# Performance work log

Measured on AMD Instinct MI355X. Metric: run time of the kernel, lower is better.

## Reference

```python
import jax, jax.numpy as jnp
import numpy as np

B, S, D = 1, 2048, 4096
H, KV, HD = 32, 8, 128          # n_heads, n_kv_heads, head_dim
NREP = H // KV                  # 4
SCALE = 1.0 / np.sqrt(HD).astype(np.float32)
ROPE_THETA = 10000.0


def setup_inputs() -> dict:
    key = jax.random.key(0)
    kx, kq, kk, kv, ko = jax.random.split(key, 5)
    x = jax.random.normal(kx, (B, S, D), jnp.float32)
    # precomputed rotary embeddings: (S, HD//2, 2) = (cos, sin)
    inv_freq = 1.0 / (ROPE_THETA ** (np.arange(0, HD, 2, dtype=np.float64) / HD))
    ang = np.outer(np.arange(S, dtype=np.float64), inv_freq)
    freqs_cis = jnp.asarray(np.stack([np.cos(ang), np.sin(ang)], axis=-1), jnp.float32)
    # additive causal mask
    mask = jnp.triu(jnp.full((S, S), -1e9, jnp.float32), k=1)
    std = 0.02
    wq = jax.random.normal(kq, (H * HD, D), jnp.float32) * std   # torch Linear layout (out, in)
    wk = jax.random.normal(kk, (KV * HD, D), jnp.float32) * std
    wv = jax.random.normal(kv, (KV * HD, D), jnp.float32) * std
    wo = jax.random.normal(ko, (D, H * HD), jnp.float32) * std
    return {"x": x, "freqs_cis": freqs_cis, "mask": mask,
            "wq": wq, "wk": wk, "wv": wv, "wo": wo}


def _apply_rope(t, fc):
    # t: [B, S, h, HD]; fc: [S, HD//2, 2] (cos, sin). Pairs adjacent dims as complex.
    b, s, h, hd = t.shape
    tr = t.reshape(b, s, h, hd // 2, 2)
    cos = fc[None, :, None, :, 0]
    sin = fc[None, :, None, :, 1]
    re = tr[..., 0] * cos - tr[..., 1] * sin
    im = tr[..., 0] * sin + tr[..., 1] * cos
    return jnp.stack([re, im], axis=-1).reshape(b, s, h, hd)


def reference(x, freqs_cis, mask, wq, wk, wv, wo):
    q = (x @ wq.T).reshape(B, S, H, HD)
    k = (x @ wk.T).reshape(B, S, KV, HD)
    v = (x @ wv.T).reshape(B, S, KV, HD)
    q = _apply_rope(q, freqs_cis)
    k = _apply_rope(k, freqs_cis)
    # GQA: head h = g * NREP + r attends to kv group g (same math as repeat_kv)
    qg = q.reshape(B, S, KV, NREP, HD)
    scores = jnp.einsum('bsgrd,btgd->bgrst', qg, k) * SCALE  # [B,KV,NREP,S,S]
    scores = scores + mask
    probs = jax.nn.softmax(scores.astype(jnp.float32), axis=-1).astype(q.dtype)
    out = jnp.einsum('bgrst,btgd->bsgrd', probs, v).reshape(B, S, H * HD)
    return out @ wo.T
```

## Files before the change

kernel.cpp:

```cpp
#include <hip/hip_runtime.h>
#include <stdint.h>

#define SCALE_F 0.08838834764831845f
#define LOG2E_F 1.4426950408889634f
#define QS_F (SCALE_F * LOG2E_F)

typedef __bf16 bf16x8_t __attribute__((ext_vector_type(8)));
typedef unsigned short u16x8 __attribute__((ext_vector_type(8)));
typedef float f32x4 __attribute__((ext_vector_type(4)));
typedef float f32x16 __attribute__((ext_vector_type(16)));

__device__ __forceinline__ unsigned short f2bf(float f) {
  unsigned int u = __float_as_uint(f);
  unsigned int r = ((u >> 16) & 1u) + 0x7FFFu;
  return (unsigned short)((u + r) >> 16);
}
__device__ __forceinline__ float bf2f(unsigned short s) {
  return __uint_as_float(((unsigned int)s) << 16);
}
__device__ __forceinline__ f32x4 mfma16(u16x8 a, u16x8 b, f32x4 c) {
  return __builtin_amdgcn_mfma_f32_16x16x32_bf16(
      __builtin_bit_cast(bf16x8_t, a), __builtin_bit_cast(bf16x8_t, b), c, 0, 0, 0);
}
__device__ __forceinline__ f32x16 mfma32(u16x8 a, u16x8 b, f32x16 c) {
  return __builtin_amdgcn_mfma_f32_32x32x16_bf16(
      __builtin_bit_cast(bf16x8_t, a), __builtin_bit_cast(bf16x8_t, b), c, 0, 0, 0);
}
__device__ __forceinline__ unsigned int cvtpk(float lo, float hi) {
  unsigned int r;
  asm("v_cvt_pk_bf16_f32 %0, %1, %2" : "=v"(r) : "v"(lo), "v"(hi));
  return r;
}
__device__ __forceinline__ float exp2_hw(float x) {
  float r;
  asm("v_exp_f32 %0, %1" : "=v"(r) : "v"(x));
  return r;
}
__device__ __forceinline__ void gload_lds16(const void* g, void* l) {
  __builtin_amdgcn_global_load_lds((const __attribute__((address_space(1))) void*)g,
                                   (__attribute__((address_space(3))) void*)l, 16, 0, 0);
}

__global__ void cvt_all(const float* __restrict__ x, const float* __restrict__ wq,
                        const float* __restrict__ wk, const float* __restrict__ wv,
                        const float* __restrict__ wo, unsigned short* __restrict__ xb,
                        unsigned short* __restrict__ wfus, unsigned short* __restrict__ wob) {
  const size_t M = 1024 * 1024;
  int b = blockIdx.x;
  const float* src;
  unsigned short* dst;
  int rb;
  if (b < 4096)       { src = x;  dst = xb;            rb = b; }
  else if (b < 12288) { src = wq; dst = wfus;          rb = b - 4096; }
  else if (b < 14336) { src = wk; dst = wfus + 16 * M; rb = b - 12288; }
  else if (b < 16384) { src = wv; dst = wfus + 20 * M; rb = b - 14336; }
  else                { src = wo; dst = wob;           rb = b - 16384; }
  size_t i = (size_t)rb * 2048 + threadIdx.x * 8;
  float4 v0 = *(const float4*)(src + i);
  float4 v1 = *(const float4*)(src + i + 4);
  uint4 o;
  o.x = (unsigned int)f2bf(v0.x) | ((unsigned int)f2bf(v0.y) << 16);
  o.y = (unsigned int)f2bf(v0.z) | ((unsigned int)f2bf(v0.w) << 16);
  o.z = (unsigned int)f2bf(v1.x) | ((unsigned int)f2bf(v1.y) << 16);
  o.w = (unsigned int)f2bf(v1.z) | ((unsigned int)f2bf(v1.w) << 16);
  *(uint4*)(dst + i) = o;
}

__global__ void kvtile(const unsigned short* __restrict__ QKV, const float* __restrict__ fc,
                       unsigned short* __restrict__ Ktil, unsigned short* __restrict__ Vtil) {
  __shared__ unsigned short vlds[32 * 128];
  int b0 = blockIdx.x;
  int tid = threadIdx.x;
  if (b0 < 512) {
    int b = b0, kvg = b >> 6, kvt = b & 63;
#pragma unroll
    for (int cc = 0; cc < 2; ++cc) {
      int c = tid + cc * 256;
      int s = c >> 5, r = c & 31;
      int key = kvt * 32 + r;
      u16x8 v = *(const u16x8*)&QKV[(size_t)key * 6144 + 4096 + kvg * 128 + s * 8];
      unsigned int o[4];
#pragma unroll
      for (int t = 0; t < 4; ++t) {
        int m = s * 4 + t;
        float cs = fc[(key * 64 + m) * 2];
        float sn = fc[(key * 64 + m) * 2 + 1];
        float a = bf2f((unsigned short)v[2 * t]), bb = bf2f((unsigned short)v[2 * t + 1]);
        o[t] = (unsigned int)f2bf(a * cs - bb * sn) |
               ((unsigned int)f2bf(a * sn + bb * cs) << 16);
      }
      *(uint4*)&Ktil[(size_t)b * 4096 + c * 8] = make_uint4(o[0], o[1], o[2], o[3]);
    }
  } else {
    int b = b0 - 512, kvg = b >> 6, kvt = b & 63;
#pragma unroll
    for (int cc = 0; cc < 2; ++cc) {
      int cl = tid + cc * 256;
      int r = cl >> 4, q = cl & 15;
      *(uint4*)&vlds[r * 128 + q * 8] =
          *(const uint4*)&QKV[(size_t)(kvt * 32 + r) * 6144 + 5120 + kvg * 128 + q * 8];
    }
    __syncthreads();
#pragma unroll
    for (int cc = 0; cc < 2; ++cc) {
      int c = tid + cc * 256;
      int v = c >> 7, hd = c & 127;
      unsigned short o[8];
#pragma unroll
      for (int t = 0; t < 8; ++t) o[t] = vlds[(v * 8 + t) * 128 + hd];
      *(uint4*)&Vtil[(size_t)b * 4096 + c * 8] = *(uint4*)o;
    }
  }
}

__global__ __launch_bounds__(512, 2) void gemm_qkv(const unsigned short* __restrict__ A,
                                                   const unsigned short* __restrict__ BT,
                                                   unsigned short* __restrict__ C) {
  const int K = 4096, N = 6144;
  __shared__ __align__(16) unsigned short smem[2 * 28672];
  const int tid = threadIdx.x;
  const int w = tid >> 6, l = tid & 63;
  const int wm = w >> 2, wn = w & 3;
  const int c16 = l & 15, h4 = l >> 4;
  const int wg = ((int)blockIdx.x & 7) * 32 + ((int)blockIdx.x >> 3);
  const int m0 = (wg & 7) << 8, n0 = (wg >> 3) * 192;

  int growA[4], gcolA[4], growB[3], gcolB[3];
#pragma unroll
  for (int p = 0; p < 4; ++p) {
    int c = p * 512 + tid, ll = c & 63;
    growA[p] = ((c >> 6) & 15) * 16 + (ll & 15);
    gcolA[p] = (c >> 10) * 32 + ((ll >> 4) << 3);
  }
#pragma unroll
  for (int p = 0; p < 3; ++p) {
    int c = p * 512 + tid, ll = c & 63, f6 = c >> 6;
    int kc = (f6 >= 12) ? 1 : 0;
    growB[p] = (f6 - 12 * kc) * 16 + (ll & 15);
    gcolB[p] = kc * 32 + ((ll >> 4) << 3);
  }
  auto stageA = [&](int e, int ks, int p) {
    gload_lds16(A + (size_t)(m0 + growA[p]) * K + ks + gcolA[p],
                &smem[e * 28672 + (p * 512 + tid) * 8]);
  };
  auto stageB = [&](int e, int ks, int p) {
    gload_lds16(BT + (size_t)(n0 + growB[p]) * K + ks + gcolB[p],
                &smem[e * 28672 + 16384 + (p * 512 + tid) * 8]);
  };

  f32x4 acc[2][4][3];
#pragma unroll
  for (int mh = 0; mh < 2; ++mh)
#pragma unroll
    for (int mf = 0; mf < 4; ++mf)
#pragma unroll
      for (int nf = 0; nf < 3; ++nf)
#pragma unroll
        for (int r = 0; r < 4; ++r) acc[mh][mf][nf][r] = 0.f;

  stageA(0, 0, 0); stageA(0, 0, 1); stageB(0, 0, 0); stageB(0, 0, 1);
  stageA(0, 0, 2); stageA(0, 0, 3); stageB(0, 0, 2);
  asm volatile("s_waitcnt vmcnt(3)" ::: "memory");
  __builtin_amdgcn_sched_barrier(0);
  asm volatile("s_barrier" ::: "memory");

  const int nt = K >> 6;
  u16x8 bfr[3];
  for (int t = 0; t < nt; ++t) {
    const int d = t & 1, e = d ^ 1;
    const int dA = d * 28672, dB = dA + 16384;
    const int ks = ((t + 1 < nt) ? t + 1 : t) << 6;
#pragma unroll
    for (int p = 0; p < 4; ++p) {
      const int kc = p >> 1, mh = p & 1;
      u16x8 af[4];
#pragma unroll
      for (int mf = 0; mf < 4; ++mf)
        af[mf] = *(const u16x8*)&smem[dA + ((kc * 16 + wm * 8 + mh * 4 + mf) * 64 + l) * 8];
      if (mh == 0) {
#pragma unroll
        for (int nf = 0; nf < 3; ++nf)
          bfr[nf] = *(const u16x8*)&smem[dB + ((kc * 12 + wn * 3 + nf) * 64 + l) * 8];
      }
      if (p == 0)      { stageA(e, ks, 0); stageA(e, ks, 1); }
      else if (p == 1) { stageB(e, ks, 0); stageB(e, ks, 1); }
      else if (p == 2) { stageA(e, ks, 2); stageA(e, ks, 3); }
      else             { stageB(e, ks, 2); }
      asm volatile("s_barrier" ::: "memory");
      asm volatile("s_waitcnt lgkmcnt(0)" ::: "memory");
      __builtin_amdgcn_sched_barrier(0);
      __builtin_amdgcn_s_setprio(1);
#pragma unroll
      for (int mf = 0; mf < 4; ++mf)
#pragma unroll
        for (int nf = 0; nf < 3; ++nf)
          acc[mh][mf][nf] = mfma16(af[mf], bfr[nf], acc[mh][mf][nf]);
      __builtin_amdgcn_s_setprio(0);
      __builtin_amdgcn_sched_barrier(0);
      if (p == 1) asm volatile("s_waitcnt vmcnt(4)" ::: "memory");
      else if (p == 3) asm volatile("s_waitcnt vmcnt(3)" ::: "memory");
      asm volatile("s_barrier" ::: "memory");
    }
  }
  asm volatile("s_waitcnt vmcnt(0)" ::: "memory");

#pragma unroll
  for (int mh = 0; mh < 2; ++mh)
#pragma unroll
    for (int mf = 0; mf < 4; ++mf)
#pragma unroll
      for (int nf = 0; nf < 3; ++nf)
#pragma unroll
        for (int r = 0; r < 4; ++r) {
          int row = m0 + wm * 128 + mh * 64 + mf * 16 + h4 * 4 + r;
          int col = n0 + wn * 48 + nf * 16 + c16;
          C[(size_t)row * N + col] = f2bf(acc[mh][mf][nf][r]);
        }
}

__global__ __launch_bounds__(512, 2) void gemm_o(const unsigned short* __restrict__ A,
                                                 const unsigned short* __restrict__ BT,
                                                 float* __restrict__ C) {
  const int K = 4096, N = 4096;
  __shared__ __align__(16) unsigned short smem[2 * 24576];
  const int tid = threadIdx.x;
  const int w = tid >> 6, l = tid & 63;
  const int wm = w >> 2, wn = w & 3;
  const int c16 = l & 15, h4 = l >> 4;
  const int wg = ((int)blockIdx.x & 7) * 32 + ((int)blockIdx.x >> 3);
  const int m0 = (wg & 15) << 7, n0 = (wg >> 4) << 8;

  int growA[2], gcolA[2], growB[4], gcolB[4];
#pragma unroll
  for (int p = 0; p < 2; ++p) {
    int c = p * 512 + tid, ll = c & 63;
    growA[p] = ((c >> 6) & 7) * 16 + (ll & 15);
    gcolA[p] = (c >> 9) * 32 + ((ll >> 4) << 3);
  }
#pragma unroll
  for (int p = 0; p < 4; ++p) {
    int c = p * 512 + tid, ll = c & 63;
    growB[p] = ((c >> 6) & 15) * 16 + (ll & 15);
    gcolB[p] = (c >> 10) * 32 + ((ll >> 4) << 3);
  }
  auto stageA = [&](int e, int ks, int p) {
    gload_lds16(A + (size_t)(m0 + growA[p]) * K + ks + gcolA[p],
                &smem[e * 24576 + (p * 512 + tid) * 8]);
  };
  auto stageB = [&](int e, int ks, int p) {
    gload_lds16(BT + (size_t)(n0 + growB[p]) * K + ks + gcolB[p],
                &smem[e * 24576 + 8192 + (p * 512 + tid) * 8]);
  };

  f32x4 acc[4][4];
#pragma unroll
  for (int mf = 0; mf < 4; ++mf)
#pragma unroll
    for (int nc = 0; nc < 4; ++nc)
#pragma unroll
      for (int r = 0; r < 4; ++r) acc[mf][nc][r] = 0.f;

  stageA(0, 0, 0); stageB(0, 0, 0); stageB(0, 0, 1);
  stageA(0, 0, 1); stageB(0, 0, 2); stageB(0, 0, 3);
  asm volatile("s_waitcnt vmcnt(3)" ::: "memory");
  __builtin_amdgcn_sched_barrier(0);
  asm volatile("s_barrier" ::: "memory");

  const int nt = K >> 6;
  u16x8 af[4];
  for (int t = 0; t < nt; ++t) {
    const int d = t & 1, e = d ^ 1;
    const int dA = d * 24576, dB = dA + 8192;
    const int ks = ((t + 1 < nt) ? t + 1 : t) << 6;
#pragma unroll
    for (int p = 0; p < 4; ++p) {
      const int kc = p >> 1, nh = p & 1;
      if (nh == 0) {
#pragma unroll
        for (int mf = 0; mf < 4; ++mf)
          af[mf] = *(const u16x8*)&smem[dA + ((kc * 8 + wm * 4 + mf) * 64 + l) * 8];
      }
      u16x8 bfr[2];
#pragma unroll
      for (int nf = 0; nf < 2; ++nf)
        bfr[nf] = *(const u16x8*)&smem[dB + ((kc * 16 + wn * 4 + nh * 2 + nf) * 64 + l) * 8];
      if (p == 0)      { stageA(e, ks, 0); stageB(e, ks, 0); }
      else if (p == 1) { stageB(e, ks, 1); }
      else if (p == 2) { stageA(e, ks, 1); stageB(e, ks, 2); }
      else             { stageB(e, ks, 3); }
      asm volatile("s_barrier" ::: "memory");
      asm volatile("s_waitcnt lgkmcnt(0)" ::: "memory");
      __builtin_amdgcn_sched_barrier(0);
      __builtin_amdgcn_s_setprio(1);
#pragma unroll
      for (int mf = 0; mf < 4; ++mf)
#pragma unroll
        for (int nf = 0; nf < 2; ++nf)
          acc[mf][nh * 2 + nf] = mfma16(af[mf], bfr[nf], acc[mf][nh * 2 + nf]);
      __builtin_amdgcn_s_setprio(0);
      __builtin_amdgcn_sched_barrier(0);
      if (p == 1 || p == 3) asm volatile("s_waitcnt vmcnt(3)" ::: "memory");
      asm volatile("s_barrier" ::: "memory");
    }
  }
  asm volatile("s_waitcnt vmcnt(0)" ::: "memory");

#pragma unroll
  for (int mf = 0; mf < 4; ++mf)
#pragma unroll
    for (int nc = 0; nc < 4; ++nc)
#pragma unroll
      for (int r = 0; r < 4; ++r) {
        int row = m0 + wm * 64 + mf * 16 + h4 * 4 + r;
        int col = n0 + wn * 64 + nc * 16 + c16;
        C[(size_t)row * N + col] = acc[mf][nc][r];
      }
}

__global__ __launch_bounds__(256) void attnk(const unsigned short* __restrict__ Q,
                                             const float* __restrict__ fc,
                                             const unsigned short* __restrict__ Ktil,
                                             const unsigned short* __restrict__ Vtil,
                                             unsigned short* __restrict__ Ao) {
  __shared__ __align__(16) unsigned short Kbuf[2][4096];
  __shared__ __align__(16) unsigned short Vbuf[2][4096];
  const int tid = threadIdx.x;
  const int w = tid >> 6, l = tid & 63;
  const int q31 = l & 31, hi = l >> 5;
  const int b = blockIdx.x;
  const int kvg = b & 7;
  const int qg = 63 - (b >> 3);
  const int head = kvg * 4 + w;
  const int qrow = qg * 32 + q31;

  u16x8 qf[8];
#pragma unroll
  for (int kc = 0; kc < 8; ++kc) {
    u16x8 raw = *(const u16x8*)&Q[(size_t)qrow * 6144 + head * 128 + kc * 16 + hi * 8];
    int mi = qrow * 64 + kc * 8 + hi * 4;
    float4 cA = *(const float4*)&fc[(size_t)mi * 2];
    float4 cB = *(const float4*)&fc[(size_t)mi * 2 + 4];
    float cs[4] = {cA.x, cA.z, cB.x, cB.z};
    float sn[4] = {cA.y, cA.w, cB.y, cB.w};
    union { unsigned int u[4]; u16x8 v; } pk;
#pragma unroll
    for (int j = 0; j < 4; ++j) {
      float a = bf2f((unsigned short)raw[2 * j]);
      float bb = bf2f((unsigned short)raw[2 * j + 1]);
      pk.u[j] = (unsigned int)f2bf((a * cs[j] - bb * sn[j]) * QS_F) |
                ((unsigned int)f2bf((a * sn[j] + bb * cs[j]) * QS_F) << 16);
    }
    qf[kc] = pk.v;
  }

  f32x16 accO[4];
#pragma unroll
  for (int f = 0; f < 4; ++f)
#pragma unroll
    for (int r = 0; r < 16; ++r) accO[f][r] = 0.f;
  float m_run = -1e30f, l_run = 0.f;

  const unsigned short* ktb = Ktil + (size_t)kvg * 64 * 4096;
  const unsigned short* vtb = Vtil + (size_t)kvg * 64 * 4096;
  auto STAGE = [&](int d, int t) {
    const unsigned short* ks = ktb + (size_t)t * 4096 + w * 1024 + l * 8;
    const unsigned short* vs = vtb + (size_t)t * 4096 + w * 1024 + l * 8;
    gload_lds16(ks, &Kbuf[d][w * 1024 + l * 8]);
    gload_lds16(ks + 512, &Kbuf[d][w * 1024 + 512 + l * 8]);
    gload_lds16(vs, &Vbuf[d][w * 1024 + l * 8]);
    gload_lds16(vs + 512, &Vbuf[d][w * 1024 + 512 + l * 8]);
  };

  STAGE(0, 0);
  int cur = 0;
  for (int kvt = 0; kvt <= qg; ++kvt) {
    __builtin_amdgcn_s_barrier();
    __builtin_amdgcn_sched_barrier(0);
    if (kvt < qg) {
      STAGE(cur ^ 1, kvt + 1);
      asm volatile("s_waitcnt vmcnt(4)" ::: "memory");
    } else {
      asm volatile("s_waitcnt vmcnt(0)" ::: "memory");
    }
    __builtin_amdgcn_s_barrier();
    __builtin_amdgcn_sched_barrier(0);

    f32x16 s;
#pragma unroll
    for (int r = 0; r < 16; ++r) s[r] = 0.f;
#pragma unroll
    for (int kc = 0; kc < 8; ++kc) {
      u16x8 kf = *(const u16x8*)&Kbuf[cur][((2 * kc + hi) * 32 + q31) * 8];
      s = mfma32(kf, qf[kc], s);
    }

    if (kvt == qg) {
#pragma unroll
      for (int r = 0; r < 16; ++r) {
        int key = (r & 3) + 8 * (r >> 2) + 4 * hi;
        if (key > q31) s[r] = -1e30f;
      }
    }

    float pm = s[0];
#pragma unroll
    for (int r = 1; r < 16; ++r) pm = fmaxf(pm, s[r]);
    pm = fmaxf(pm, __shfl_xor(pm, 32, 64));
    if (!__all(pm - m_run <= 8.f)) {
      float mn = fmaxf(m_run, pm);
      float al = exp2_hw(m_run - mn);
      m_run = mn;
      l_run *= al;
#pragma unroll
      for (int f = 0; f < 4; ++f)
#pragma unroll
        for (int r = 0; r < 16; ++r) accO[f][r] *= al;
    }
    float p[16], ls = 0.f;
#pragma unroll
    for (int r = 0; r < 16; ++r) { p[r] = exp2_hw(s[r] - m_run); ls += p[r]; }
    l_run += ls + __shfl_xor(ls, 32, 64);

    unsigned int wv[8], wp[8];
#pragma unroll
    for (int i = 0; i < 8; ++i) wv[i] = cvtpk(p[2 * i], p[2 * i + 1]);
#pragma unroll
    for (int i = 0; i < 8; ++i) wp[i] = (unsigned int)__shfl_xor((int)wv[i], 32, 64);
    union { unsigned int u[4]; u16x8 v; } pf0, pf1;
    pf0.u[0] = hi ? wp[2] : wv[0];
    pf0.u[1] = hi ? wp[3] : wv[1];
    pf0.u[2] = hi ? wv[2] : wp[0];
    pf0.u[3] = hi ? wv[3] : wp[1];
    pf1.u[0] = hi ? wp[6] : wv[4];
    pf1.u[1] = hi ? wp[7] : wv[5];
    pf1.u[2] = hi ? wv[6] : wp[4];
    pf1.u[3] = hi ? wv[7] : wp[5];

#pragma unroll
    for (int f = 0; f < 4; ++f) {
      u16x8 vf0 = *(const u16x8*)&Vbuf[cur][((hi) * 128 + f * 32 + q31) * 8];
      u16x8 vf1 = *(const u16x8*)&Vbuf[cur][((2 + hi) * 128 + f * 32 + q31) * 8];
      accO[f] = mfma32(vf0, pf0.v, accO[f]);
      accO[f] = mfma32(vf1, pf1.v, accO[f]);
    }
    cur ^= 1;
  }

  float linv = 1.0f / l_run;
  unsigned short* orow = Ao + (size_t)qrow * 4096 + head * 128;
#pragma unroll
  for (int f = 0; f < 4; ++f)
#pragma unroll
    for (int g4 = 0; g4 < 4; ++g4) {
      unsigned int lo = (unsigned int)f2bf(accO[f][g4 * 4 + 0] * linv) |
                        ((unsigned int)f2bf(accO[f][g4 * 4 + 1] * linv) << 16);
      unsigned int hi2 = (unsigned int)f2bf(accO[f][g4 * 4 + 2] * linv) |
                         ((unsigned int)f2bf(accO[f][g4 * 4 + 3] * linv) << 16);
      *(uint2*)(orow + f * 32 + 8 * g4 + 4 * hi) = make_uint2(lo, hi2);
    }
}

extern "C" void kernel_launch(void* const* d_in, const int* in_sizes, int n_in,
                              void* d_out, int out_size, void* d_ws, size_t ws_size,
                              hipStream_t stream) {
  (void)in_sizes; (void)n_in; (void)out_size; (void)ws_size;
  const float* x  = (const float*)d_in[0];
  const float* fc = (const float*)d_in[1];
  const float* wq = (const float*)d_in[3];
  const float* wk = (const float*)d_in[4];
  const float* wv = (const float*)d_in[5];
  const float* wo = (const float*)d_in[6];

  const size_t M = 1024 * 1024;
  unsigned short* xb   = (unsigned short*)d_ws;
  unsigned short* wfus = xb   + 8 * M;
  unsigned short* wob  = wfus + 24 * M;
  unsigned short* QKV  = wob  + 16 * M;
  unsigned short* Ktil = QKV  + 12 * M;
  unsigned short* Vtil = Ktil + 2 * M;
  unsigned short* Ab   = xb;

  cvt_all<<<dim3(24576), 256, 0, stream>>>(x, wq, wk, wv, wo, xb, wfus, wob);

  gemm_qkv<<<dim3(256), 512, 0, stream>>>(xb, wfus, QKV);

  kvtile<<<dim3(1024), 256, 0, stream>>>(QKV, fc, Ktil, Vtil);

  attnk<<<dim3(512), 256, 0, stream>>>(QKV, fc, Ktil, Vtil, Ab);

  gemm_o<<<dim3(256), 512, 0, stream>>>(Ab, wob, (float*)d_out);
}
```

Before: 342.8 us.

## Process two KV tiles per pipeline stage and interleave causal block ordering

Result: faster. 328.4 us (-4.2%).

```diff
diff --git a/kernel.cpp b/kernel.cpp
--- a/kernel.cpp
+++ b/kernel.cpp
@@ -322,14 +322,15 @@
                                              const unsigned short* __restrict__ Ktil,
                                              const unsigned short* __restrict__ Vtil,
                                              unsigned short* __restrict__ Ao) {
-  __shared__ __align__(16) unsigned short Kbuf[2][4096];
-  __shared__ __align__(16) unsigned short Vbuf[2][4096];
+  __shared__ __align__(16) unsigned short Kbuf[2][8192];
+  __shared__ __align__(16) unsigned short Vbuf[2][8192];
   const int tid = threadIdx.x;
   const int w = tid >> 6, l = tid & 63;
   const int q31 = l & 31, hi = l >> 5;
   const int b = blockIdx.x;
   const int kvg = b & 7;
-  const int qg = 63 - (b >> 3);
+  const int j = b >> 3;
+  const int qg = (j < 32) ? (63 - 2 * j) : (2 * (j - 32));
   const int head = kvg * 4 + w;
   const int qrow = qg * 32 + q31;
 
@@ -344,11 +345,11 @@
     float sn[4] = {cA.y, cA.w, cB.y, cB.w};
     union { unsigned int u[4]; u16x8 v; } pk;
 #pragma unroll
-    for (int j = 0; j < 4; ++j) {
-      float a = bf2f((unsigned short)raw[2 * j]);
-      float bb = bf2f((unsigned short)raw[2 * j + 1]);
-      pk.u[j] = (unsigned int)f2bf((a * cs[j] - bb * sn[j]) * QS_F) |
-                ((unsigned int)f2bf((a * sn[j] + bb * cs[j]) * QS_F) << 16);
+    for (int jj = 0; jj < 4; ++jj) {
+      float a = bf2f((unsigned short)raw[2 * jj]);
+      float bb = bf2f((unsigned short)raw[2 * jj + 1]);
+      pk.u[jj] = (unsigned int)f2bf((a * cs[jj] - bb * sn[jj]) * QS_F) |
+                 ((unsigned int)f2bf((a * sn[jj] + bb * cs[jj]) * QS_F) << 16);
     }
     qf[kc] = pk.v;
   }
@@ -362,49 +363,67 @@
 
   const unsigned short* ktb = Ktil + (size_t)kvg * 64 * 4096;
   const unsigned short* vtb = Vtil + (size_t)kvg * 64 * 4096;
-  auto STAGE = [&](int d, int t) {
-    const unsigned short* ks = ktb + (size_t)t * 4096 + w * 1024 + l * 8;
-    const unsigned short* vs = vtb + (size_t)t * 4096 + w * 1024 + l * 8;
-    gload_lds16(ks, &Kbuf[d][w * 1024 + l * 8]);
-    gload_lds16(ks + 512, &Kbuf[d][w * 1024 + 512 + l * 8]);
-    gload_lds16(vs, &Vbuf[d][w * 1024 + l * 8]);
-    gload_lds16(vs + 512, &Vbuf[d][w * 1024 + 512 + l * 8]);
+  auto STAGE = [&](int d, int s) {
+    const unsigned short* ks = ktb + (size_t)s * 8192 + w * 2048 + l * 8;
+    const unsigned short* vs = vtb + (size_t)s * 8192 + w * 2048 + l * 8;
+#pragma unroll
+    for (int q = 0; q < 4; ++q) {
+      gload_lds16(ks + q * 512, &Kbuf[d][w * 2048 + q * 512 + l * 8]);
+      gload_lds16(vs + q * 512, &Vbuf[d][w * 2048 + q * 512 + l * 8]);
+    }
   };
 
+  const int nst = (qg >> 1) + 1;
   STAGE(0, 0);
   int cur = 0;
-  for (int kvt = 0; kvt <= qg; ++kvt) {
+  for (int st = 0; st < nst; ++st) {
     __builtin_amdgcn_s_barrier();
     __builtin_amdgcn_sched_barrier(0);
-    if (kvt < qg) {
-      STAGE(cur ^ 1, kvt + 1);
-      asm volatile("s_waitcnt vmcnt(4)" ::: "memory");
+    if (st + 1 < nst) {
+      STAGE(cur ^ 1, st + 1);
+      asm volatile("s_waitcnt vmcnt(8)" ::: "memory");
     } else {
       asm volatile("s_waitcnt vmcnt(0)" ::: "memory");
     }
     __builtin_amdgcn_s_barrier();
     __builtin_amdgcn_sched_barrier(0);
 
-    f32x16 s;
-#pragma unroll
-    for (int r = 0; r < 16; ++r) s[r] = 0.f;
+    f32x16 s0, s1;
+#pragma unroll
+    for (int r = 0; r < 16; ++r) { s0[r] = 0.f; s1[r] = 0.f; }
 #pragma unroll
     for (int kc = 0; kc < 8; ++kc) {
       u16x8 kf = *(const u16x8*)&Kbuf[cur][((2 * kc + hi) * 32 + q31) * 8];
-      s = mfma32(kf, qf[kc], s);
-    }
-
-    if (kvt == qg) {
-#pragma unroll
-      for (int r = 0; r < 16; ++r) {
-        int key = (r & 3) + 8 * (r >> 2) + 4 * hi;
-        if (key > q31) s[r] = -1e30f;
-      }
-    }
-
-    float pm = s[0];
-#pragma unroll
-    for (int r = 1; r < 16; ++r) pm = fmaxf(pm, s[r]);
+      s0 = mfma32(kf, qf[kc], s0);
+    }
+#pragma unroll
+    for (int kc = 0; kc < 8; ++kc) {
+      u16x8 kf = *(const u16x8*)&Kbuf[cur][4096 + ((2 * kc + hi) * 32 + q31) * 8];
+      s1 = mfma32(kf, qf[kc], s1);
+    }
+
+    if (st == nst - 1) {
+      if ((qg & 1) == 0) {
+#pragma unroll
+        for (int r = 0; r < 16; ++r) {
+          int key = (r & 3) + 8 * (r >> 2) + 4 * hi;
+          if (key > q31) s0[r] = -1e30f;
+          s1[r] = -1e30f;
+        }
+      } else {
+#pragma unroll
+        for (int r = 0; r < 16; ++r) {
+          int key = (r & 3) + 8 * (r >> 2) + 4 * hi;
+          if (key > q31) s1[r] = -1e30f;
+        }
+      }
+    }
+
+    float pm = s0[0];
+#pragma unroll
+    for (int r = 1; r < 16; ++r) pm = fmaxf(pm, s0[r]);
+#pragma unroll
+    for (int r = 0; r < 16; ++r) pm = fmaxf(pm, s1[r]);
     pm = fmaxf(pm, __shfl_xor(pm, 32, 64));
     if (!__all(pm - m_run <= 8.f)) {
       float mn = fmaxf(m_run, pm);
@@ -416,33 +435,61 @@
 #pragma unroll
         for (int r = 0; r < 16; ++r) accO[f][r] *= al;
     }
-    float p[16], ls = 0.f;
-#pragma unroll
-    for (int r = 0; r < 16; ++r) { p[r] = exp2_hw(s[r] - m_run); ls += p[r]; }
-    l_run += ls + __shfl_xor(ls, 32, 64);
-
-    unsigned int wv[8], wp[8];
-#pragma unroll
-    for (int i = 0; i < 8; ++i) wv[i] = cvtpk(p[2 * i], p[2 * i + 1]);
-#pragma unroll
-    for (int i = 0; i < 8; ++i) wp[i] = (unsigned int)__shfl_xor((int)wv[i], 32, 64);
-    union { unsigned int u[4]; u16x8 v; } pf0, pf1;
-    pf0.u[0] = hi ? wp[2] : wv[0];
-    pf0.u[1] = hi ? wp[3] : wv[1];
-    pf0.u[2] = hi ? wv[2] : wp[0];
-    pf0.u[3] = hi ? wv[3] : wp[1];
-    pf1.u[0] = hi ? wp[6] : wv[4];
-    pf1.u[1] = hi ? wp[7] : wv[5];
-    pf1.u[2] = hi ? wv[6] : wp[4];
-    pf1.u[3] = hi ? wv[7] : wp[5];
-
-#pragma unroll
-    for (int f = 0; f < 4; ++f) {
-      u16x8 vf0 = *(const u16x8*)&Vbuf[cur][((hi) * 128 + f * 32 + q31) * 8];
-      u16x8 vf1 = *(const u16x8*)&Vbuf[cur][((2 + hi) * 128 + f * 32 + q31) * 8];
-      accO[f] = mfma32(vf0, pf0.v, accO[f]);
-      accO[f] = mfma32(vf1, pf1.v, accO[f]);
-    }
+
+    float lsum = 0.f;
+    {
+      float p[16];
+#pragma unroll
+      for (int r = 0; r < 16; ++r) { p[r] = exp2_hw(s0[r] - m_run); lsum += p[r]; }
+      unsigned int wv[8], wp[8];
+#pragma unroll
+      for (int i = 0; i < 8; ++i) wv[i] = cvtpk(p[2 * i], p[2 * i + 1]);
+#pragma unroll
+      for (int i = 0; i < 8; ++i) wp[i] = (unsigned int)__shfl_xor((int)wv[i], 32, 64);
+      union { unsigned int u[4]; u16x8 v; } pf0, pf1;
+      pf0.u[0] = hi ? wp[2] : wv[0];
+      pf0.u[1] = hi ? wp[3] : wv[1];
+      pf0.u[2] = hi ? wv[2] : wp[0];
+      pf0.u[3] = hi ? wv[3] : wp[1];
+      pf1.u[0] = hi ? wp[6] : wv[4];
+      pf1.u[1] = hi ? wp[7] : wv[5];
+      pf1.u[2] = hi ? wv[6] : wp[4];
+      pf1.u[3] = hi ? wv[7] : wp[5];
+#pragma unroll
+      for (int f = 0; f < 4; ++f) {
+        u16x8 vf0 = *(const u16x8*)&Vbuf[cur][((hi) * 128 + f * 32 + q31) * 8];
+        u16x8 vf1 = *(const u16x8*)&Vbuf[cur][((2 + hi) * 128 + f * 32 + q31) * 8];
+        accO[f] = mfma32(vf0, pf0.v, accO[f]);
+        accO[f] = mfma32(vf1, pf1.v, accO[f]);
+      }
+    }
+    {
+      float p[16];
+#pragma unroll
+      for (int r = 0; r < 16; ++r) { p[r] = exp2_hw(s1[r] - m_run); lsum += p[r]; }
+      unsigned int wv[8], wp[8];
+#pragma unroll
+      for (int i = 0; i < 8; ++i) wv[i] = cvtpk(p[2 * i], p[2 * i + 1]);
+#pragma unroll
+      for (int i = 0; i < 8; ++i) wp[i] = (unsigned int)__shfl_xor((int)wv[i], 32, 64);
+      union { unsigned int u[4]; u16x8 v; } pf0, pf1;
+      pf0.u[0] = hi ? wp[2] : wv[0];
+      pf0.u[1] = hi ? wp[3] : wv[1];
+      pf0.u[2] = hi ? wv[2] : wp[0];
+      pf0.u[3] = hi ? wv[3] : wp[1];
+      pf1.u[0] = hi ? wp[6] : wv[4];
+      pf1.u[1] = hi ? wp[7] : wv[5];
+      pf1.u[2] = hi ? wv[6] : wp[4];
+      pf1.u[3] = hi ? wv[7] : wp[5];
+#pragma unroll
+      for (int f = 0; f < 4; ++f) {
+        u16x8 vf0 = *(const u16x8*)&Vbuf[cur][4096 + ((hi) * 128 + f * 32 + q31) * 8];
+        u16x8 vf1 = *(const u16x8*)&Vbuf[cur][4096 + ((2 + hi) * 128 + f * 32 + q31) * 8];
+        accO[f] = mfma32(vf0, pf0.v, accO[f]);
+        accO[f] = mfma32(vf1, pf1.v, accO[f]);
+      }
+    }
+    l_run += lsum + __shfl_xor(lsum, 32, 64);
     cur ^= 1;
   }
 
```
